# Optimization experiments

Measured on AMD Instinct MI355X. Metric: run time of the kernel, lower is better.

## Reference

```python
import jax, jax.numpy as jnp
import numpy as np

SPARSITY = 0.8  # fraction of weights zeroed (random unstructured mask)

def setup_inputs() -> dict:
    key = jax.random.key(0)
    k1, k2, k3, k4 = jax.random.split(key, 4)
    B, S, D_IN, D_OUT = 4, 2048, 4096, 4096
    x = jax.random.normal(k1, (B, S, D_IN), dtype=jnp.float32)
    weight = jax.random.normal(k2, (D_OUT, D_IN), dtype=jnp.float32) * 0.02
    bias = jax.random.normal(k3, (D_OUT,), dtype=jnp.float32) * 0.02
    # fixed binary mask: keep with prob (1 - sparsity)
    mask = (jax.random.uniform(k4, (D_OUT, D_IN)) >= SPARSITY).astype(jnp.float32)
    return {"x": x, "weight": weight, "bias": bias, "mask": mask}

def reference(x, weight, bias, mask):
    # w = weight * mask; y = x @ w.T + b   (F.linear semantics)
    w = weight * mask                      # [O, I]
    y = jnp.einsum('bsi,oi->bso', x, w)    # [B, S, O]
    return y + bias
```

## Files before the change

### kernel.cpp

```cpp
#include <hip/hip_runtime.h>
#include <hip/hip_bf16.h>
#include <stdint.h>

#define M_DIM 8192
#define N_DIM 4096
#define K_DIM 4096

#define BM 256
#define BN 256
#define BK 64
#define NT (K_DIM / BK)

typedef __attribute__((ext_vector_type(8))) __bf16 bf16x8;
typedef __attribute__((ext_vector_type(4))) float floatx4;

__device__ inline unsigned f2b(float f) {
    union { float f; unsigned u; } v; v.f = f;
    return (v.u + 0x7FFFu + ((v.u >> 16) & 1u)) >> 16;
}
__device__ inline unsigned pk2(float lo, float hi) {
    return (f2b(lo) & 0xFFFFu) | (f2b(hi) << 16);
}

__device__ inline void async_load16(const void* g, void* l) {
    __builtin_amdgcn_global_load_lds(
        (const __attribute__((address_space(1))) unsigned int*)(unsigned long long)g,
        (__attribute__((address_space(3))) unsigned int*)(unsigned int)(unsigned long long)l,
        16, 0, 0);
}

#define SFENCE() asm volatile("" ::: "memory")

#define CVT_GRID 2048
#define CVT_XBLK 1152
__global__ __launch_bounds__(256)
void cvt_all(const float4* __restrict__ x, const float4* __restrict__ w,
             const float4* __restrict__ m, uint4* __restrict__ xb,
             uint4* __restrict__ wb, int nx8, int nw8) {
    if ((int)blockIdx.x < CVT_XBLK) {
        int i = blockIdx.x * 256 + threadIdx.x;
        const int stride = CVT_XBLK * 256;
        for (; i < nx8; i += stride) {
            float4 a = x[2 * i], b = x[2 * i + 1];
            uint4 o;
            o.x = pk2(a.x, a.y); o.y = pk2(a.z, a.w);
            o.z = pk2(b.x, b.y); o.w = pk2(b.z, b.w);
            xb[i] = o;
        }
    } else {
        int i = ((int)blockIdx.x - CVT_XBLK) * 256 + threadIdx.x;
        const int stride = (CVT_GRID - CVT_XBLK) * 256;
        for (; i < nw8; i += stride) {
            float4 w0 = w[2 * i], w1 = w[2 * i + 1];
            float4 m0 = m[2 * i], m1 = m[2 * i + 1];
            uint4 o;
            o.x = pk2(w0.x * m0.x, w0.y * m0.y);
            o.y = pk2(w0.z * m0.z, w0.w * m0.w);
            o.z = pk2(w1.x * m1.x, w1.y * m1.y);
            o.w = pk2(w1.z * m1.z, w1.w * m1.w);
            wb[i] = o;
        }
    }
}

__global__ __launch_bounds__(512, 2)
void gemm_8phase(const __hip_bfloat16* __restrict__ A,
                 const __hip_bfloat16* __restrict__ B,
                 const float* __restrict__ bias,
                 float* __restrict__ C) {
    __shared__ __hip_bfloat16 As[2][2][128][64];
    __shared__ __hip_bfloat16 Bs[2][2][128][64];

    const int t    = threadIdx.x;
    const int lane = t & 63;
    const int wave = t >> 6;
    const int wm   = wave >> 2;
    const int wn   = wave & 3;
    const int lm   = lane & 15;
    const int h4   = lane >> 4;

    const int wg = (blockIdx.x & 7) * 64 + (blockIdx.x >> 3);
    const int m0 = (wg >> 4) * BM;
    const int n0 = (wg & 15) * BN;

    const int srow = t >> 3;
    const int schk = t & 7;
    const int sx   = schk ^ (srow & 7);

    const __hip_bfloat16* gA[2][2];
    const __hip_bfloat16* gB[2][2];
#pragma unroll
    for (int h = 0; h < 2; h++)
#pragma unroll
        for (int r = 0; r < 2; r++) {
            gA[h][r] = A + (size_t)(m0 + h * 128 + r * 64 + srow) * K_DIM + sx * 8;
            gB[h][r] = B + (size_t)(n0 + h * 128 + r * 64 + srow) * K_DIM + sx * 8;
        }

#define STAGE_A(b, h, r, tt) \
    async_load16(gA[h][r] + (tt) * BK, &As[b][h][(r) * 64 + srow][schk * 8])
#define STAGE_B(b, h, r, tt) \
    async_load16(gB[h][r] + (tt) * BK, &Bs[b][h][(r) * 64 + srow][schk * 8])

    const int cs0 = ((h4)     ^ (lm & 7)) * 8;
    const int cs1 = ((4 + h4) ^ (lm & 7)) * 8;

#define LDA(b, i, kk) \
    (*(const bf16x8*)&As[b][wm][(i) * 16 + lm][(kk) ? cs1 : cs0])
#define LDB(b, j, kk) \
    (*(const bf16x8*)&Bs[b][wn >> 1][(wn & 1) * 64 + (j) * 16 + lm][(kk) ? cs1 : cs0])

    floatx4 acc[8][4] = {};
    bf16x8 af[4], bfr[4][2];

    STAGE_A(0, 0, 0, 0); STAGE_A(0, 1, 0, 0);
    STAGE_A(0, 0, 1, 0); STAGE_A(0, 1, 1, 0);
    STAGE_B(0, 0, 0, 0); STAGE_B(0, 0, 1, 0);
    STAGE_B(0, 1, 0, 0); STAGE_B(0, 1, 1, 0);
    STAGE_A(1, 0, 0, 1); STAGE_A(1, 1, 0, 1);
    STAGE_B(1, 0, 0, 1); STAGE_B(1, 0, 1, 1);
    STAGE_B(1, 1, 0, 1); STAGE_B(1, 1, 1, 1);
    asm volatile("s_waitcnt vmcnt(6)" ::: "memory");
    __builtin_amdgcn_s_barrier();
    SFENCE();

    for (int s = 0; s < NT; ++s) {
        const int b  = s & 1;
        const int nb = b ^ 1;

#pragma unroll
        for (int i = 0; i < 4; i++) af[i] = LDA(b, i, 0);
#pragma unroll
        for (int j = 0; j < 4; j++) bfr[j][0] = LDB(b, j, 0);
        if (s + 1 < NT) { STAGE_A(nb, 0, 1, s + 1); STAGE_A(nb, 1, 1, s + 1); }
        asm volatile("s_waitcnt lgkmcnt(4)" ::: "memory");
        SFENCE(); __builtin_amdgcn_s_barrier();
        asm volatile("s_waitcnt lgkmcnt(0)" ::: "memory");
        __builtin_amdgcn_s_setprio(1);
#pragma unroll
        for (int i = 0; i < 4; i++)
#pragma unroll
            for (int j = 0; j < 4; j++)
                acc[i][j] = __builtin_amdgcn_mfma_f32_16x16x32_bf16(
                    af[i], bfr[j][0], acc[i][j], 0, 0, 0);
        __builtin_amdgcn_s_setprio(0);
        SFENCE(); __builtin_amdgcn_s_barrier(); SFENCE();

#pragma unroll
        for (int i = 0; i < 4; i++) af[i] = LDA(b, i, 1);
#pragma unroll
        for (int j = 0; j < 4; j++) bfr[j][1] = LDB(b, j, 1);
        asm volatile("s_waitcnt lgkmcnt(4)" ::: "memory");
        SFENCE(); __builtin_amdgcn_s_barrier();
        asm volatile("s_waitcnt lgkmcnt(0)" ::: "memory");
        __builtin_amdgcn_s_setprio(1);
#pragma unroll
        for (int i = 0; i < 4; i++)
#pragma unroll
            for (int j = 0; j < 4; j++)
                acc[i][j] = __builtin_amdgcn_mfma_f32_16x16x32_bf16(
                    af[i], bfr[j][1], acc[i][j], 0, 0, 0);
        __builtin_amdgcn_s_setprio(0);
        SFENCE(); __builtin_amdgcn_s_barrier(); SFENCE();

#pragma unroll
        for (int i = 0; i < 4; i++) af[i] = LDA(b, 4 + i, 0);
        if (s + 2 < NT) {
            STAGE_A(b, 0, 0, s + 2); STAGE_A(b, 1, 0, s + 2);
            STAGE_B(b, 0, 0, s + 2); STAGE_B(b, 0, 1, s + 2);
        }
        SFENCE(); __builtin_amdgcn_s_barrier();
        asm volatile("s_waitcnt lgkmcnt(0)" ::: "memory");
        __builtin_amdgcn_s_setprio(1);
#pragma unroll
        for (int i = 0; i < 4; i++)
#pragma unroll
            for (int j = 0; j < 4; j++)
                acc[4 + i][j] = __builtin_amdgcn_mfma_f32_16x16x32_bf16(
                    af[i], bfr[j][0], acc[4 + i][j], 0, 0, 0);
        __builtin_amdgcn_s_setprio(0);
        SFENCE(); __builtin_amdgcn_s_barrier(); SFENCE();

#pragma unroll
        for (int i = 0; i < 4; i++) af[i] = LDA(b, 4 + i, 1);
        if (s + 2 < NT) { STAGE_B(b, 1, 0, s + 2); STAGE_B(b, 1, 1, s + 2); }
        asm volatile("s_waitcnt lgkmcnt(0)" ::: "memory");
        __builtin_amdgcn_s_setprio(1);
#pragma unroll
        for (int i = 0; i < 4; i++)
#pragma unroll
            for (int j = 0; j < 4; j++)
                acc[4 + i][j] = __builtin_amdgcn_mfma_f32_16x16x32_bf16(
                    af[i], bfr[j][1], acc[4 + i][j], 0, 0, 0);
        __builtin_amdgcn_s_setprio(0);
        if (s + 2 < NT) asm volatile("s_waitcnt vmcnt(6)" ::: "memory");
        else            asm volatile("s_waitcnt vmcnt(0)" ::: "memory");
        SFENCE(); __builtin_amdgcn_s_barrier(); SFENCE();
    }

    float bv[4];
#pragma unroll
    for (int j = 0; j < 4; j++)
        bv[j] = bias[n0 + wn * 64 + j * 16 + lm];
    const int row_base = m0 + wm * 128 + h4 * 4;
    const int col_base = n0 + wn * 64 + lm;
#pragma unroll
    for (int i = 0; i < 8; i++)
#pragma unroll
        for (int j = 0; j < 4; j++) {
            const int col = col_base + j * 16;
#pragma unroll
            for (int r = 0; r < 4; r++)
                C[(size_t)(row_base + i * 16 + r) * N_DIM + col] =
                    acc[i][j][r] + bv[j];
        }
}

extern "C" void kernel_launch(void* const* d_in, const int* in_sizes, int n_in,
                              void* d_out, int out_size, void* d_ws, size_t ws_size,
                              hipStream_t stream) {
    const float* x    = (const float*)d_in[0];
    const float* w    = (const float*)d_in[1];
    const float* bias = (const float*)d_in[2];
    const float* mask = (const float*)d_in[3];
    float* out = (float*)d_out;

    __hip_bfloat16* xb = (__hip_bfloat16*)d_ws;
    __hip_bfloat16* wb = xb + (size_t)M_DIM * K_DIM;

    cvt_all<<<dim3(CVT_GRID), dim3(256), 0, stream>>>(
        (const float4*)x, (const float4*)w, (const float4*)mask,
        (uint4*)xb, (uint4*)wb, M_DIM * K_DIM / 8, N_DIM * K_DIM / 8);
    gemm_8phase<<<dim3(512), dim3(512), 0, stream>>>(xb, wb, bias, out);
}
```

Measured before the change: 531.3 us.

## Restructure GEMM K-tile phases to split N halves and unroll by two

Reorders each K-tile's four compute phases. A fragments now cover both k-halves at once and the four B columns are split into two pairs, so each phase does 16 MFMAs over the full BK=64 instead of one k-half. The main loop is unrolled by two with constant buffer indices, and the async stage issue points shift (A stages move to phase two, B stages to phases three and four). It also retunes the convert kernel's split between x blocks and weight blocks. The intent is to cut LDS reload traffic and indexing overhead, at the cost of more fragment registers and different wait timing.

New measurement: 527.2 us. No clear change (-0.8%).

```diff
diff --git a/kernel.cpp b/kernel.cpp
--- a/kernel.cpp
+++ b/kernel.cpp
@@ -32,7 +32,7 @@
 #define SFENCE() asm volatile("" ::: "memory")
 
 #define CVT_GRID 2048
-#define CVT_XBLK 1152
+#define CVT_XBLK 1120
 __global__ __launch_bounds__(256)
 void cvt_all(const float4* __restrict__ x, const float4* __restrict__ w,
              const float4* __restrict__ m, uint4* __restrict__ xb,
@@ -98,9 +98,9 @@
         }
 
 #define STAGE_A(b, h, r, tt) \
-    async_load16(gA[h][r] + (tt) * BK, &As[b][h][(r) * 64 + srow][schk * 8])
+    async_load16(gA[h][r] + (size_t)(tt) * BK, &As[b][h][(r) * 64 + srow][schk * 8])
 #define STAGE_B(b, h, r, tt) \
-    async_load16(gB[h][r] + (tt) * BK, &Bs[b][h][(r) * 64 + srow][schk * 8])
+    async_load16(gB[h][r] + (size_t)(tt) * BK, &Bs[b][h][(r) * 64 + srow][schk * 8])
 
     const int cs0 = ((h4)     ^ (lm & 7)) * 8;
     const int cs1 = ((4 + h4) ^ (lm & 7)) * 8;
@@ -111,7 +111,53 @@
     (*(const bf16x8*)&Bs[b][wn >> 1][(wn & 1) * 64 + (j) * 16 + lm][(kk) ? cs1 : cs0])
 
     floatx4 acc[8][4] = {};
-    bf16x8 af[4], bfr[4][2];
+    bf16x8 af[4][2], b01[2][2], b23[2][2];
+
+#define MFMA16(bi, bj, B_)                                                    \
+    __builtin_amdgcn_s_setprio(1);                                            \
+    _Pragma("unroll") for (int i = 0; i < 4; i++)                             \
+    _Pragma("unroll") for (int j = 0; j < 2; j++)                             \
+    _Pragma("unroll") for (int kk = 0; kk < 2; kk++)                          \
+        acc[(bi) + i][(bj) + j] = __builtin_amdgcn_mfma_f32_16x16x32_bf16(    \
+            af[i][kk], B_[j][kk], acc[(bi) + i][(bj) + j], 0, 0, 0);          \
+    __builtin_amdgcn_s_setprio(0);
+
+#define KTILE(b, nb, ss)                                                      \
+  { const int s_ = (ss);                                                      \
+                                               \
+    _Pragma("unroll") for (int i = 0; i < 4; i++) {                           \
+        af[i][0] = LDA(b, i, 0); af[i][1] = LDA(b, i, 1); }                   \
+    _Pragma("unroll") for (int j = 0; j < 2; j++) {                           \
+        b01[j][0] = LDB(b, j, 0); b01[j][1] = LDB(b, j, 1); }                 \
+    if (s_ + 1 < NT) { STAGE_A(nb, 0, 1, s_ + 1); STAGE_A(nb, 1, 1, s_ + 1); }\
+    asm volatile("s_waitcnt lgkmcnt(8)" ::: "memory");                        \
+    SFENCE(); __builtin_amdgcn_s_barrier();                                   \
+    asm volatile("s_waitcnt lgkmcnt(0)" ::: "memory");                        \
+    MFMA16(0, 0, b01)                                                         \
+    SFENCE(); __builtin_amdgcn_s_barrier(); SFENCE();                         \
+                                               \
+    _Pragma("unroll") for (int j = 0; j < 2; j++) {                           \
+        b23[j][0] = LDB(b, 2 + j, 0); b23[j][1] = LDB(b, 2 + j, 1); }         \
+    if (s_ + 2 < NT) { STAGE_A(b, 0, 0, s_ + 2); STAGE_A(b, 1, 0, s_ + 2); }  \
+    SFENCE(); __builtin_amdgcn_s_barrier();                                   \
+    asm volatile("s_waitcnt lgkmcnt(0)" ::: "memory");                        \
+    MFMA16(0, 2, b23)                                                         \
+    SFENCE(); __builtin_amdgcn_s_barrier(); SFENCE();                         \
+                                               \
+    _Pragma("unroll") for (int i = 0; i < 4; i++) {                           \
+        af[i][0] = LDA(b, 4 + i, 0); af[i][1] = LDA(b, 4 + i, 1); }           \
+    if (s_ + 2 < NT) { STAGE_B(b, 0, 0, s_ + 2); STAGE_B(b, 0, 1, s_ + 2); }  \
+    SFENCE(); __builtin_amdgcn_s_barrier();                                   \
+    asm volatile("s_waitcnt lgkmcnt(0)" ::: "memory");                        \
+    MFMA16(4, 0, b01)                                                         \
+    SFENCE(); __builtin_amdgcn_s_barrier(); SFENCE();                         \
+                                               \
+    if (s_ + 2 < NT) { STAGE_B(b, 1, 0, s_ + 2); STAGE_B(b, 1, 1, s_ + 2); }  \
+    MFMA16(4, 2, b23)                                                         \
+    if (s_ + 2 < NT) asm volatile("s_waitcnt vmcnt(6)" ::: "memory");         \
+    else             asm volatile("s_waitcnt vmcnt(0)" ::: "memory");         \
+    SFENCE(); __builtin_amdgcn_s_barrier(); SFENCE();                         \
+  }
 
     STAGE_A(0, 0, 0, 0); STAGE_A(0, 1, 0, 0);
     STAGE_A(0, 0, 1, 0); STAGE_A(0, 1, 1, 0);
@@ -124,78 +170,9 @@
     __builtin_amdgcn_s_barrier();
     SFENCE();
 
-    for (int s = 0; s < NT; ++s) {
-        const int b  = s & 1;
-        const int nb = b ^ 1;
-
-#pragma unroll
-        for (int i = 0; i < 4; i++) af[i] = LDA(b, i, 0);
-#pragma unroll
-        for (int j = 0; j < 4; j++) bfr[j][0] = LDB(b, j, 0);
-        if (s + 1 < NT) { STAGE_A(nb, 0, 1, s + 1); STAGE_A(nb, 1, 1, s + 1); }
-        asm volatile("s_waitcnt lgkmcnt(4)" ::: "memory");
-        SFENCE(); __builtin_amdgcn_s_barrier();
-        asm volatile("s_waitcnt lgkmcnt(0)" ::: "memory");
-        __builtin_amdgcn_s_setprio(1);
-#pragma unroll
-        for (int i = 0; i < 4; i++)
-#pragma unroll
-            for (int j = 0; j < 4; j++)
-                acc[i][j] = __builtin_amdgcn_mfma_f32_16x16x32_bf16(
-                    af[i], bfr[j][0], acc[i][j], 0, 0, 0);
-        __builtin_amdgcn_s_setprio(0);
-        SFENCE(); __builtin_amdgcn_s_barrier(); SFENCE();
-
-#pragma unroll
-        for (int i = 0; i < 4; i++) af[i] = LDA(b, i, 1);
-#pragma unroll
-        for (int j = 0; j < 4; j++) bfr[j][1] = LDB(b, j, 1);
-        asm volatile("s_waitcnt lgkmcnt(4)" ::: "memory");
-        SFENCE(); __builtin_amdgcn_s_barrier();
-        asm volatile("s_waitcnt lgkmcnt(0)" ::: "memory");
-        __builtin_amdgcn_s_setprio(1);
-#pragma unroll
-        for (int i = 0; i < 4; i++)
-#pragma unroll
-            for (int j = 0; j < 4; j++)
-                acc[i][j] = __builtin_amdgcn_mfma_f32_16x16x32_bf16(
-                    af[i], bfr[j][1], acc[i][j], 0, 0, 0);
-        __builtin_amdgcn_s_setprio(0);
-        SFENCE(); __builtin_amdgcn_s_barrier(); SFENCE();
-
-#pragma unroll
-        for (int i = 0; i < 4; i++) af[i] = LDA(b, 4 + i, 0);
-        if (s + 2 < NT) {
-            STAGE_A(b, 0, 0, s + 2); STAGE_A(b, 1, 0, s + 2);
-            STAGE_B(b, 0, 0, s + 2); STAGE_B(b, 0, 1, s + 2);
-        }
-        SFENCE(); __builtin_amdgcn_s_barrier();
-        asm volatile("s_waitcnt lgkmcnt(0)" ::: "memory");
-        __builtin_amdgcn_s_setprio(1);
-#pragma unroll
-        for (int i = 0; i < 4; i++)
-#pragma unroll
-            for (int j = 0; j < 4; j++)
-                acc[4 + i][j] = __builtin_amdgcn_mfma_f32_16x16x32_bf16(
-                    af[i], bfr[j][0], acc[4 + i][j], 0, 0, 0);
-        __builtin_amdgcn_s_setprio(0);
-        SFENCE(); __builtin_amdgcn_s_barrier(); SFENCE();
-
-#pragma unroll
-        for (int i = 0; i < 4; i++) af[i] = LDA(b, 4 + i, 1);
-        if (s + 2 < NT) { STAGE_B(b, 1, 0, s + 2); STAGE_B(b, 1, 1, s + 2); }
-        asm volatile("s_waitcnt lgkmcnt(0)" ::: "memory");
-        __builtin_amdgcn_s_setprio(1);
-#pragma unroll
-        for (int i = 0; i < 4; i++)
-#pragma unroll
-            for (int j = 0; j < 4; j++)
-                acc[4 + i][j] = __builtin_amdgcn_mfma_f32_16x16x32_bf16(
-                    af[i], bfr[j][1], acc[4 + i][j], 0, 0, 0);
-        __builtin_amdgcn_s_setprio(0);
-        if (s + 2 < NT) asm volatile("s_waitcnt vmcnt(6)" ::: "memory");
-        else            asm volatile("s_waitcnt vmcnt(0)" ::: "memory");
-        SFENCE(); __builtin_amdgcn_s_barrier(); SFENCE();
+    for (int s = 0; s < NT; s += 2) {
+        KTILE(0, 1, s)
+        KTILE(1, 0, s + 1)
     }
 
     float bv[4];
```
